# Kernel tuning notes

Hardware: AMD Instinct MI355X
Metric: run time of the kernel (lower is better)

## Reference

```python
import jax, jax.numpy as jnp
import numpy as np

B, H, S, D = 2, 16, 2048, 64

def setup_inputs() -> dict:
    key = jax.random.key(0)
    kq, kk, kv = jax.random.split(key, 3)
    Q = jax.random.normal(kq, (B, H, S, D), dtype=jnp.float32)
    K = jax.random.normal(kk, (B, H, S, D), dtype=jnp.float32)
    V = jax.random.normal(kv, (B, H, S, D), dtype=jnp.float32)
    # causal mask, broadcastable over batch/head dims (True = keep)
    mask = jnp.tril(jnp.ones((S, S), dtype=jnp.bool_))
    return {"Q": Q, "K": K, "V": V, "mask": mask}

def reference(Q, K, V, mask):
    scale = jax.lax.rsqrt(jnp.float32(Q.shape[-1]))
    # [b, h, q, k] attention logits
    at = jnp.einsum('bhqd,bhkd->bhqk', Q, K) * scale
    at = jnp.where(mask, at, -jnp.inf)
    # manual numerically-stable softmax (matches SoftMax module)
    x_max = jnp.max(at, axis=-1, keepdims=True)
    x_exp = jnp.exp(at - x_max)
    scores = x_exp / jnp.sum(x_exp, axis=-1, keepdims=True)
    return jnp.einsum('bhqk,bhkd->bhqd', scores, V)
```

## Files before the change

kernel.cpp:

```cpp
#include <hip/hip_runtime.h>
#include <math.h>

typedef __attribute__((ext_vector_type(8))) short bf16x8;
typedef __attribute__((ext_vector_type(8))) short s16x8;
typedef __attribute__((ext_vector_type(4))) short s16x4;
typedef __attribute__((ext_vector_type(4))) int   i32x4;
typedef __attribute__((ext_vector_type(4))) float f32x4;
typedef __attribute__((ext_vector_type(16))) float f32x16;

namespace {
constexpr int kS   = 2048;
constexpr int kD   = 64;
constexpr int kBH  = 32;
constexpr int kT   = kS / 64;
constexpr int PPAD = 72;
constexpr float kScaleLog2e = 0.125f * 1.44269504088896340736f;
}

__device__ __forceinline__ short f2bf(float f) {
    union { float f; unsigned u; } c; c.f = f;
    unsigned r = c.u + 0x7fffu + ((c.u >> 16) & 1u);
    return (short)(r >> 16);
}

__device__ __forceinline__ s16x8 pack8(const float4& a, const float4& b) {
    s16x8 r;
    r[0] = f2bf(a.x); r[1] = f2bf(a.y); r[2] = f2bf(a.z); r[3] = f2bf(a.w);
    r[4] = f2bf(b.x); r[5] = f2bf(b.y); r[6] = f2bf(b.z); r[7] = f2bf(b.w);
    return r;
}

__device__ __forceinline__ float hexp2(float x) {
    float r;
    asm("v_exp_f32 %0, %1" : "=v"(r) : "v"(x));
    return r;
}

__device__ __forceinline__ unsigned cvtpk(float lo, float hi_) {
    unsigned r;
    asm("v_cvt_pk_bf16_f32 %0, %1, %2" : "=v"(r) : "v"(lo), "v"(hi_));
    return r;
}
__device__ __forceinline__ void plswap(unsigned& a, unsigned& b) {
    asm("v_permlane32_swap_b32 %0, %1" : "+v"(a), "+v"(b));
}

__global__ __launch_bounds__(256)
void prepack(const float* __restrict__ K, const float* __restrict__ V,
             short* __restrict__ wsK, short* __restrict__ wsVT)
{
    __shared__ float vt[64][65];
    const int tid = threadIdx.x;
    const int kb  = blockIdx.x;
    const int bh  = blockIdx.y;
    const int r   = tid >> 2;
    const int s   = tid & 3;
    const int c0  = s * 16;

    const size_t grow = ((size_t)bh * kS + (size_t)kb * 64 + r) * kD + c0;
    const size_t tbase = ((size_t)bh * kT + kb) * 4096;

    {
        const float4* kr = (const float4*)(K + grow);
        float4 a = kr[0], b = kr[1], c = kr[2], d = kr[3];
        const int kt = r >> 5, ql = r & 31;
        short* out = wsK + tbase + (size_t)((s * 2 + kt) * 64) * 8;
        *(s16x8*)(out + (size_t)ql * 8)        = pack8(a, b);
        *(s16x8*)(out + (size_t)(32 + ql) * 8) = pack8(c, d);
    }
    {
        const float4* vr = (const float4*)(V + grow);
        float4 a = vr[0], b = vr[1], c = vr[2], d = vr[3];
        float t[16] = {a.x,a.y,a.z,a.w, b.x,b.y,b.z,b.w,
                       c.x,c.y,c.z,c.w, d.x,d.y,d.z,d.w};
        #pragma unroll
        for (int jj = 0; jj < 16; ++jj) vt[r][c0 + jj] = t[jj];
    }
    __syncthreads();
    {
        const int d     = tid >> 2;
        const int slice = tid & 3;
        const int k0    = slice * 16;
        const int dt = d >> 5, ql = d & 31;
        s16x8 g0, g1;
        #pragma unroll
        for (int jj = 0; jj < 8; ++jj) g0[jj] = f2bf(vt[k0 + jj][d]);
        #pragma unroll
        for (int jj = 0; jj < 8; ++jj) g1[jj] = f2bf(vt[k0 + 8 + jj][d]);
        short* out = wsVT + tbase + (size_t)((slice * 2 + dt) * 64) * 8;
        *(s16x8*)(out + (size_t)ql * 8)        = g0;
        *(s16x8*)(out + (size_t)(32 + ql) * 8) = g1;
    }
}

__global__ __launch_bounds__(64)
void attn_v11(const float* __restrict__ Q, const short* __restrict__ wsK,
              const short* __restrict__ wsVT, float* __restrict__ O)
{
    const int lane = threadIdx.x & 63;
    const int ql   = lane & 31;
    const int hi   = lane >> 5;

    const int n    = (int)blockIdx.x;
    const int xcd  = n & 7;
    const int rest = n >> 3;
    const int bh   = xcd * 4 + (rest >> 5);
    const int p    = rest & 31;

    const char* Kroot = (const char*)wsK + (size_t)bh * kT * 8192;
    const char* Vroot = (const char*)wsVT + (size_t)bh * kT * 8192;

    f32x16 z16;
    #pragma unroll
    for (int c = 0; c < 16; ++c) z16[c] = 0.f;

    bf16x8 onesA;
    #pragma unroll
    for (int i = 0; i < 8; ++i) onesA[i] = (short)0x3F80;

    auto loadK = [&](int kb, bf16x8 (&kf)[8]) {
        const char* kp = Kroot + (size_t)kb * 8192 + lane * 16;
        #pragma unroll
        for (int i = 0; i < 8; ++i)
            kf[i] = *(const bf16x8*)(kp + i * 1024);
    };

    #pragma unroll 1
    for (int sidx = 0; sidx < 2; ++sidx) {
        const int qs   = sidx == 0 ? 63 - p : p;
        const int T    = (qs >> 1) + 1;
        const int qrow = qs * 32 + ql;

        const float* Qr = Q + ((size_t)bh * kS + qrow) * kD;
        bf16x8 qf[4];
        #pragma unroll
        for (int s = 0; s < 4; ++s) {
            const float4 a = *(const float4*)(Qr + s * 16 + hi * 8);
            const float4 b = *(const float4*)(Qr + s * 16 + hi * 8 + 4);
            bf16x8 f;
            f[0] = f2bf(a.x * kScaleLog2e); f[1] = f2bf(a.y * kScaleLog2e);
            f[2] = f2bf(a.z * kScaleLog2e); f[3] = f2bf(a.w * kScaleLog2e);
            f[4] = f2bf(b.x * kScaleLog2e); f[5] = f2bf(b.y * kScaleLog2e);
            f[6] = f2bf(b.z * kScaleLog2e); f[7] = f2bf(b.w * kScaleLog2e);
            qf[s] = f;
        }

        f32x16 o[2] = {z16, z16};
        f32x16 lacc = z16;

        bf16x8 kA[8], kB[8];
        loadK(0, kA);

        auto tile = [&](bf16x8 (&kcur)[8], bf16x8 (&knxt)[8], int kb) {
            bf16x8 vf[8];
            {
                const char* vp = Vroot + (size_t)kb * 8192 + lane * 16;
                #pragma unroll
                for (int i = 0; i < 8; ++i)
                    vf[i] = *(const bf16x8*)(vp + i * 1024);
            }

            f32x16 sacc[2];
            #pragma unroll
            for (int kt = 0; kt < 2; ++kt) {
                sacc[kt] = __builtin_amdgcn_mfma_f32_32x32x16_bf16(
                    kcur[kt], qf[0], z16, 0, 0, 0);
                #pragma unroll
                for (int s = 1; s < 4; ++s)
                    sacc[kt] = __builtin_amdgcn_mfma_f32_32x32x16_bf16(
                        kcur[s * 2 + kt], qf[s], sacc[kt], 0, 0, 0);
            }

            if (kb + 1 < T) loadK(kb + 1, knxt);

            if (kb == T - 1) {
                #pragma unroll
                for (int kt = 0; kt < 2; ++kt) {
                    const int kbase = kb * 64 + kt * 32 + 4 * hi;
                    #pragma unroll
                    for (int c = 0; c < 16; ++c) {
                        const int kg = kbase + (c & 3) + 8 * (c >> 2);
                        if (kg > qrow) sacc[kt][c] = -1e30f;
                    }
                }
            }

            #pragma unroll
            for (int kt = 0; kt < 2; ++kt)
                #pragma unroll
                for (int c = 0; c < 16; ++c)
                    sacc[kt][c] = hexp2(sacc[kt][c]);

            #pragma unroll
            for (int kt = 0; kt < 2; ++kt) {
                unsigned w8[8];
                #pragma unroll
                for (int i = 0; i < 8; ++i)
                    w8[i] = cvtpk(sacc[kt][2 * i], sacc[kt][2 * i + 1]);
                #pragma unroll
                for (int s = 0; s < 2; ++s) {
                    unsigned A0 = w8[4 * s + 0], B0 = w8[4 * s + 2];
                    unsigned A1 = w8[4 * s + 1], B1 = w8[4 * s + 3];
                    plswap(A0, B0);
                    plswap(A1, B1);
                    i32x4 wv;
                    wv[0] = (int)A0; wv[1] = (int)A1;
                    wv[2] = (int)B0; wv[3] = (int)B1;
                    const bf16x8 pv = __builtin_bit_cast(bf16x8, wv);
                    #pragma unroll
                    for (int dt = 0; dt < 2; ++dt)
                        o[dt] = __builtin_amdgcn_mfma_f32_32x32x16_bf16(
                            vf[(kt * 2 + s) * 2 + dt], pv, o[dt], 0, 0, 0);
                    lacc = __builtin_amdgcn_mfma_f32_32x32x16_bf16(
                        onesA, pv, lacc, 0, 0, 0);
                }
            }
        };

        int kb = 0;
        #pragma unroll 1
        while (true) {
            tile(kA, kB, kb);
            if (++kb == T) break;
            tile(kB, kA, kb);
            if (++kb == T) break;
        }

        const float inv = 1.0f / lacc[0];
        float* Ob = O + ((size_t)bh * kS + qrow) * kD;
        #pragma unroll
        for (int dt = 0; dt < 2; ++dt)
            #pragma unroll
            for (int t = 0; t < 4; ++t) {
                float4 v;
                v.x = o[dt][4 * t + 0] * inv;
                v.y = o[dt][4 * t + 1] * inv;
                v.z = o[dt][4 * t + 2] * inv;
                v.w = o[dt][4 * t + 3] * inv;
                *(float4*)(Ob + dt * 32 + 4 * hi + 8 * t) = v;
            }
    }
}

__global__ __launch_bounds__(256)
void attn_mfma(const float* __restrict__ Q, const float* __restrict__ K,
               const float* __restrict__ V, float* __restrict__ O)
{
    __shared__ short Klds[64 * PPAD];
    __shared__ short VTlds[64 * PPAD];
    __shared__ short Plds[4 * 16 * PPAD];

    const int tid  = threadIdx.x;
    const int lane = tid & 63;
    const int w    = tid >> 6;
    const int lo   = lane & 15;
    const int hi   = lane >> 4;
    const int qt = (int)gridDim.x - 1 - (int)blockIdx.x;
    const int bh = blockIdx.y;
    const size_t hbase = (size_t)bh * kS * kD;

    const float* Qr = Q + hbase + (size_t)(qt * 64 + w * 16 + lo) * kD;
    bf16x8 qfrag[2];
    #pragma unroll
    for (int dc = 0; dc < 2; ++dc) {
        const float4 a = *(const float4*)(Qr + dc * 32 + hi * 8);
        const float4 b = *(const float4*)(Qr + dc * 32 + hi * 8 + 4);
        bf16x8 f;
        f[0] = f2bf(a.x * kScaleLog2e); f[1] = f2bf(a.y * kScaleLog2e);
        f[2] = f2bf(a.z * kScaleLog2e); f[3] = f2bf(a.w * kScaleLog2e);
        f[4] = f2bf(b.x * kScaleLog2e); f[5] = f2bf(b.y * kScaleLog2e);
        f[6] = f2bf(b.z * kScaleLog2e); f[7] = f2bf(b.w * kScaleLog2e);
        qfrag[dc] = f;
    }

    const f32x4 zero4 = {0.f, 0.f, 0.f, 0.f};
    f32x4 o[4] = {zero4, zero4, zero4, zero4};
    float m_[4] = {-1e30f, -1e30f, -1e30f, -1e30f};
    float l_[4] = {0.f, 0.f, 0.f, 0.f};
    const int sr = tid >> 2;
    const int sc = (tid & 3) * 16;
    const float* Kg = K + hbase;
    const float* Vg = V + hbase;
    short* Pw = &Plds[w * 16 * PPAD];

    for (int kb = 0; kb <= qt; ++kb) {
        __syncthreads();
        {
            const float* krow = Kg + (size_t)(kb * 64 + sr) * kD + sc;
            const float* vrow = Vg + (size_t)(kb * 64 + sr) * kD + sc;
            #pragma unroll
            for (int i = 0; i < 4; ++i) {
                const float4 kv = ((const float4*)krow)[i];
                s16x4 ks;
                ks[0] = f2bf(kv.x); ks[1] = f2bf(kv.y);
                ks[2] = f2bf(kv.z); ks[3] = f2bf(kv.w);
                *(s16x4*)&Klds[sr * PPAD + sc + i * 4] = ks;
                const float4 vv = ((const float4*)vrow)[i];
                VTlds[(sc + i * 4 + 0) * PPAD + sr] = f2bf(vv.x);
                VTlds[(sc + i * 4 + 1) * PPAD + sr] = f2bf(vv.y);
                VTlds[(sc + i * 4 + 2) * PPAD + sr] = f2bf(vv.z);
                VTlds[(sc + i * 4 + 3) * PPAD + sr] = f2bf(vv.w);
            }
        }
        __syncthreads();

        f32x4 sacc[4] = {zero4, zero4, zero4, zero4};
        #pragma unroll
        for (int kk = 0; kk < 4; ++kk)
            #pragma unroll
            for (int dc = 0; dc < 2; ++dc) {
                const bf16x8 kf = *(const bf16x8*)(
                    &Klds[(kk * 16 + lo) * PPAD + dc * 32 + hi * 8]);
                sacc[kk] = __builtin_amdgcn_mfma_f32_16x16x32_bf16(
                    qfrag[dc], kf, sacc[kk], 0, 0, 0);
            }
        if (kb == qt) {
            #pragma unroll
            for (int kk = 0; kk < 4; ++kk)
                #pragma unroll
                for (int r = 0; r < 4; ++r)
                    if (kk * 16 + lo > w * 16 + hi * 4 + r) sacc[kk][r] = -1e30f;
        }
        float nm[4], alpha[4];
        #pragma unroll
        for (int r = 0; r < 4; ++r) {
            float v = fmaxf(fmaxf(sacc[0][r], sacc[1][r]),
                            fmaxf(sacc[2][r], sacc[3][r]));
            v = fmaxf(v, __shfl_xor(v, 1));
            v = fmaxf(v, __shfl_xor(v, 2));
            v = fmaxf(v, __shfl_xor(v, 4));
            v = fmaxf(v, __shfl_xor(v, 8));
            nm[r]    = fmaxf(v, m_[r]);
            alpha[r] = exp2f(m_[r] - nm[r]);
        }
        float p[4][4];
        #pragma unroll
        for (int kk = 0; kk < 4; ++kk)
            #pragma unroll
            for (int r = 0; r < 4; ++r)
                p[kk][r] = exp2f(sacc[kk][r] - nm[r]);
        #pragma unroll
        for (int r = 0; r < 4; ++r) {
            float s = (p[0][r] + p[1][r]) + (p[2][r] + p[3][r]);
            s += __shfl_xor(s, 1);
            s += __shfl_xor(s, 2);
            s += __shfl_xor(s, 4);
            s += __shfl_xor(s, 8);
            l_[r] = l_[r] * alpha[r] + s;
            m_[r] = nm[r];
        }
        #pragma unroll
        for (int dcB = 0; dcB < 4; ++dcB)
            #pragma unroll
            for (int r = 0; r < 4; ++r)
                o[dcB][r] *= alpha[r];
        #pragma unroll
        for (int kk = 0; kk < 4; ++kk)
            #pragma unroll
            for (int r = 0; r < 4; ++r)
                Pw[(hi * 4 + r) * PPAD + kk * 16 + lo] = f2bf(p[kk][r]);
        #pragma unroll
        for (int kc = 0; kc < 2; ++kc) {
            const bf16x8 pf = *(const bf16x8*)(&Pw[lo * PPAD + kc * 32 + hi * 8]);
            #pragma unroll
            for (int dcB = 0; dcB < 4; ++dcB) {
                const bf16x8 vf = *(const bf16x8*)(
                    &VTlds[(dcB * 16 + lo) * PPAD + kc * 32 + hi * 8]);
                o[dcB] = __builtin_amdgcn_mfma_f32_16x16x32_bf16(
                    pf, vf, o[dcB], 0, 0, 0);
            }
        }
    }
    float* Ob = O + hbase;
    #pragma unroll
    for (int r = 0; r < 4; ++r) {
        const float inv = 1.0f / l_[r];
        const size_t q = (size_t)(qt * 64 + w * 16 + hi * 4 + r);
        #pragma unroll
        for (int dcB = 0; dcB < 4; ++dcB)
            Ob[q * kD + dcB * 16 + lo] = o[dcB][r] * inv;
    }
}

extern "C" void kernel_launch(void* const* d_in, const int* in_sizes, int n_in,
                              void* d_out, int out_size, void* d_ws, size_t ws_size,
                              hipStream_t stream) {
    const float* Q = (const float*)d_in[0];
    const float* K = (const float*)d_in[1];
    const float* V = (const float*)d_in[2];
    float* out = (float*)d_out;
    (void)in_sizes; (void)n_in; (void)out_size;

    const size_t elemsK   = (size_t)kBH * kS * kD;
    const size_t need_pre = elemsK * 2 * sizeof(short);

    if (ws_size >= need_pre) {
        short* wsK  = (short*)d_ws;
        short* wsVT = wsK + elemsK;
        prepack<<<dim3(kT, kBH), 256, 0, stream>>>(K, V, wsK, wsVT);
        attn_v11<<<dim3(1024), 64, 0, stream>>>(Q, wsK, wsVT, out);
    } else {
        attn_mfma<<<dim3(kT, kBH), 256, 0, stream>>>(Q, K, V, out);
    }
}
```

Before: 52.13 us.

## Share K/V tiles across four waves via LDS with async global-to-LDS staging

Replaces the one-wave-per-block attention kernel with a 256-thread block of four waves covering 128 query rows. These waves share double-buffered K/V tiles that are loaded into LDS with global_load_lds. This cuts redundant global/L2 traffic for K and V by a factor of four and overlaps the next tile's load with compute. The cost is a __syncthreads per key tile and only 256 blocks instead of 1024. The causal mask check is also generalised per wave, because waves in a block end their causal range at different points.

```diff
diff --git a/kernel.cpp b/kernel.cpp
--- a/kernel.cpp
+++ b/kernel.cpp
@@ -43,6 +43,12 @@
 }
 __device__ __forceinline__ void plswap(unsigned& a, unsigned& b) {
     asm("v_permlane32_swap_b32 %0, %1" : "+v"(a), "+v"(b));
+}
+
+typedef const __attribute__((address_space(1))) void* gas_t;
+typedef __attribute__((address_space(3))) void* las_t;
+__device__ __forceinline__ void glds16(const void* g, void* l) {
+    __builtin_amdgcn_global_load_lds((gas_t)g, (las_t)l, 16, 0, 0);
 }
 
 __global__ __launch_bounds__(256)
@@ -93,19 +99,24 @@
     }
 }
 
-__global__ __launch_bounds__(64)
-void attn_v11(const float* __restrict__ Q, const short* __restrict__ wsK,
+__global__ __launch_bounds__(256)
+void attn_v12(const float* __restrict__ Q, const short* __restrict__ wsK,
               const short* __restrict__ wsVT, float* __restrict__ O)
 {
-    const int lane = threadIdx.x & 63;
+    __shared__ short Kst[2][4096];
+    __shared__ short Vst[2][4096];
+
+    const int tid  = threadIdx.x;
+    const int lane = tid & 63;
+    const int w    = tid >> 6;
     const int ql   = lane & 31;
     const int hi   = lane >> 5;
 
-    const int n    = (int)blockIdx.x;
-    const int xcd  = n & 7;
-    const int rest = n >> 3;
-    const int bh   = xcd * 4 + (rest >> 5);
-    const int p    = rest & 31;
+    const int n   = (int)blockIdx.x;
+    const int xcd = n & 7;
+    const int j   = n >> 3;
+    const int bh  = xcd * 4 + (j & 3);
+    const int pr  = j >> 2;
 
     const char* Kroot = (const char*)wsK + (size_t)bh * kT * 8192;
     const char* Vroot = (const char*)wsVT + (size_t)bh * kT * 8192;
@@ -118,18 +129,22 @@
     #pragma unroll
     for (int i = 0; i < 8; ++i) onesA[i] = (short)0x3F80;
 
-    auto loadK = [&](int kb, bf16x8 (&kf)[8]) {
-        const char* kp = Kroot + (size_t)kb * 8192 + lane * 16;
-        #pragma unroll
-        for (int i = 0; i < 8; ++i)
-            kf[i] = *(const bf16x8*)(kp + i * 1024);
+    auto stage = [&](int kb, int b) {
+        const char* ks = Kroot + (size_t)kb * 8192 + tid * 16;
+        const char* vs = Vroot + (size_t)kb * 8192 + tid * 16;
+        char* kl = (char*)&Kst[b][0] + tid * 16;
+        char* vl = (char*)&Vst[b][0] + tid * 16;
+        glds16(ks,        kl);
+        glds16(ks + 4096, kl + 4096);
+        glds16(vs,        vl);
+        glds16(vs + 4096, vl + 4096);
     };
 
     #pragma unroll 1
-    for (int sidx = 0; sidx < 2; ++sidx) {
-        const int qs   = sidx == 0 ? 63 - p : p;
-        const int T    = (qs >> 1) + 1;
-        const int qrow = qs * 32 + ql;
+    for (int ph = 0; ph < 2; ++ph) {
+        const int qb   = ph ? pr : (15 - pr);
+        const int T    = 2 * qb + 2;
+        const int qrow = qb * 128 + w * 32 + ql;
 
         const float* Qr = Q + ((size_t)bh * kS + qrow) * kD;
         bf16x8 qf[4];
@@ -148,32 +163,32 @@
         f32x16 o[2] = {z16, z16};
         f32x16 lacc = z16;
 
-        bf16x8 kA[8], kB[8];
-        loadK(0, kA);
-
-        auto tile = [&](bf16x8 (&kcur)[8], bf16x8 (&knxt)[8], int kb) {
-            bf16x8 vf[8];
-            {
-                const char* vp = Vroot + (size_t)kb * 8192 + lane * 16;
-                #pragma unroll
-                for (int i = 0; i < 8; ++i)
-                    vf[i] = *(const bf16x8*)(vp + i * 1024);
-            }
+        stage(0, 0);
+        __syncthreads();
+
+        #pragma unroll 1
+        for (int kb = 0; kb < T; ++kb) {
+            const int b = kb & 1;
+            if (kb + 1 < T) stage(kb + 1, b ^ 1);
+
+            const char* Kl = (const char*)&Kst[b][0] + lane * 16;
+            const char* Vl = (const char*)&Vst[b][0] + lane * 16;
 
             f32x16 sacc[2];
             #pragma unroll
             for (int kt = 0; kt < 2; ++kt) {
+                const bf16x8 k0 = *(const bf16x8*)(Kl + kt * 1024);
                 sacc[kt] = __builtin_amdgcn_mfma_f32_32x32x16_bf16(
-                    kcur[kt], qf[0], z16, 0, 0, 0);
-                #pragma unroll
-                for (int s = 1; s < 4; ++s)
+                    k0, qf[0], z16, 0, 0, 0);
+                #pragma unroll
+                for (int s = 1; s < 4; ++s) {
+                    const bf16x8 kf = *(const bf16x8*)(Kl + (s * 2 + kt) * 1024);
                     sacc[kt] = __builtin_amdgcn_mfma_f32_32x32x16_bf16(
-                        kcur[s * 2 + kt], qf[s], sacc[kt], 0, 0, 0);
-            }
-
-            if (kb + 1 < T) loadK(kb + 1, knxt);
-
-            if (kb == T - 1) {
+                        kf, qf[s], sacc[kt], 0, 0, 0);
+                }
+            }
+
+            if (kb * 64 + 63 > qrow) {
                 #pragma unroll
                 for (int kt = 0; kt < 2; ++kt) {
                     const int kbase = kb * 64 + kt * 32 + 4 * hi;
@@ -208,22 +223,18 @@
                     wv[2] = (int)B0; wv[3] = (int)B1;
                     const bf16x8 pv = __builtin_bit_cast(bf16x8, wv);
                     #pragma unroll
-                    for (int dt = 0; dt < 2; ++dt)
+                    for (int dt = 0; dt < 2; ++dt) {
+                        const bf16x8 vfr = *(const bf16x8*)(
+                            Vl + ((kt * 2 + s) * 2 + dt) * 1024);
                         o[dt] = __builtin_amdgcn_mfma_f32_32x32x16_bf16(
-                            vf[(kt * 2 + s) * 2 + dt], pv, o[dt], 0, 0, 0);
+                            vfr, pv, o[dt], 0, 0, 0);
+                    }
                     lacc = __builtin_amdgcn_mfma_f32_32x32x16_bf16(
                         onesA, pv, lacc, 0, 0, 0);
                 }
             }
-        };
-
-        int kb = 0;
-        #pragma unroll 1
-        while (true) {
-            tile(kA, kB, kb);
-            if (++kb == T) break;
-            tile(kB, kA, kb);
-            if (++kb == T) break;
+
+            __syncthreads();
         }
 
         const float inv = 1.0f / lacc[0];
@@ -239,6 +250,7 @@
                 v.w = o[dt][4 * t + 3] * inv;
                 *(float4*)(Ob + dt * 32 + 4 * hi + 8 * t) = v;
             }
+        __syncthreads();
     }
 }
 
@@ -398,7 +410,7 @@
         short* wsK  = (short*)d_ws;
         short* wsVT = wsK + elemsK;
         prepack<<<dim3(kT, kBH), 256, 0, stream>>>(K, V, wsK, wsVT);
-        attn_v11<<<dim3(1024), 64, 0, stream>>>(Q, wsK, wsVT, out);
+        attn_v12<<<dim3(256), 256, 0, stream>>>(Q, wsK, wsVT, out);
     } else {
         attn_mfma<<<dim3(kT, kBH), 256, 0, stream>>>(Q, K, V, out);
     }
```

Result: slower. 58.28 us (+11.8%).

## Software-pipeline QK^T one tile ahead and double-buffer V loads with MFMA priority

Applied to the files above, without the earlier changes.

Restructures the attention inner loop so the QK^T MFMAs for tile kb+1 are issued before the softmax and PV work of tile kb. K is now prefetched two tiles ahead and V one tile ahead, each into its own double buffer. s_setprio is raised around MFMA groups so matrix work gets issue priority over other waves. This aims to hide global-load latency and the exp/convert ALU work behind MFMA, at the cost of more VGPRs for the extra S and V buffers, which could reduce occupancy or cause spills.

```diff
diff --git a/kernel.cpp b/kernel.cpp
--- a/kernel.cpp
+++ b/kernel.cpp
@@ -94,7 +94,7 @@
 }
 
 __global__ __launch_bounds__(64)
-void attn_v11(const float* __restrict__ Q, const short* __restrict__ wsK,
+void attn_v13(const float* __restrict__ Q, const short* __restrict__ wsK,
               const short* __restrict__ wsVT, float* __restrict__ O)
 {
     const int lane = threadIdx.x & 63;
@@ -123,6 +123,12 @@
         #pragma unroll
         for (int i = 0; i < 8; ++i)
             kf[i] = *(const bf16x8*)(kp + i * 1024);
+    };
+    auto loadV = [&](int kb, bf16x8 (&vf)[8]) {
+        const char* vp = Vroot + (size_t)kb * 8192 + lane * 16;
+        #pragma unroll
+        for (int i = 0; i < 8; ++i)
+            vf[i] = *(const bf16x8*)(vp + i * 1024);
     };
 
     #pragma unroll 1
@@ -148,31 +154,21 @@
         f32x16 o[2] = {z16, z16};
         f32x16 lacc = z16;
 
-        bf16x8 kA[8], kB[8];
-        loadK(0, kA);
-
-        auto tile = [&](bf16x8 (&kcur)[8], bf16x8 (&knxt)[8], int kb) {
-            bf16x8 vf[8];
-            {
-                const char* vp = Vroot + (size_t)kb * 8192 + lane * 16;
-                #pragma unroll
-                for (int i = 0; i < 8; ++i)
-                    vf[i] = *(const bf16x8*)(vp + i * 1024);
-            }
-
-            f32x16 sacc[2];
+        auto qkt = [&](bf16x8 (&kf)[8], f32x16 (&S)[2]) {
+            __builtin_amdgcn_s_setprio(1);
             #pragma unroll
             for (int kt = 0; kt < 2; ++kt) {
-                sacc[kt] = __builtin_amdgcn_mfma_f32_32x32x16_bf16(
-                    kcur[kt], qf[0], z16, 0, 0, 0);
+                S[kt] = __builtin_amdgcn_mfma_f32_32x32x16_bf16(
+                    kf[kt], qf[0], z16, 0, 0, 0);
                 #pragma unroll
                 for (int s = 1; s < 4; ++s)
-                    sacc[kt] = __builtin_amdgcn_mfma_f32_32x32x16_bf16(
-                        kcur[s * 2 + kt], qf[s], sacc[kt], 0, 0, 0);
-            }
-
-            if (kb + 1 < T) loadK(kb + 1, knxt);
-
+                    S[kt] = __builtin_amdgcn_mfma_f32_32x32x16_bf16(
+                        kf[s * 2 + kt], qf[s], S[kt], 0, 0, 0);
+            }
+            __builtin_amdgcn_s_setprio(0);
+        };
+
+        auto finish = [&](f32x16 (&S)[2], bf16x8 (&vf)[8], int kb) {
             if (kb == T - 1) {
                 #pragma unroll
                 for (int kt = 0; kt < 2; ++kt) {
@@ -180,23 +176,22 @@
                     #pragma unroll
                     for (int c = 0; c < 16; ++c) {
                         const int kg = kbase + (c & 3) + 8 * (c >> 2);
-                        if (kg > qrow) sacc[kt][c] = -1e30f;
+                        if (kg > qrow) S[kt][c] = -1e30f;
                     }
                 }
             }
-
             #pragma unroll
             for (int kt = 0; kt < 2; ++kt)
                 #pragma unroll
                 for (int c = 0; c < 16; ++c)
-                    sacc[kt][c] = hexp2(sacc[kt][c]);
+                    S[kt][c] = hexp2(S[kt][c]);
 
             #pragma unroll
             for (int kt = 0; kt < 2; ++kt) {
                 unsigned w8[8];
                 #pragma unroll
                 for (int i = 0; i < 8; ++i)
-                    w8[i] = cvtpk(sacc[kt][2 * i], sacc[kt][2 * i + 1]);
+                    w8[i] = cvtpk(S[kt][2 * i], S[kt][2 * i + 1]);
                 #pragma unroll
                 for (int s = 0; s < 2; ++s) {
                     unsigned A0 = w8[4 * s + 0], B0 = w8[4 * s + 2];
@@ -207,22 +202,39 @@
                     wv[0] = (int)A0; wv[1] = (int)A1;
                     wv[2] = (int)B0; wv[3] = (int)B1;
                     const bf16x8 pv = __builtin_bit_cast(bf16x8, wv);
+                    __builtin_amdgcn_s_setprio(1);
                     #pragma unroll
                     for (int dt = 0; dt < 2; ++dt)
                         o[dt] = __builtin_amdgcn_mfma_f32_32x32x16_bf16(
                             vf[(kt * 2 + s) * 2 + dt], pv, o[dt], 0, 0, 0);
                     lacc = __builtin_amdgcn_mfma_f32_32x32x16_bf16(
                         onesA, pv, lacc, 0, 0, 0);
+                    __builtin_amdgcn_s_setprio(0);
                 }
             }
         };
+
+        bf16x8 kA[8], kB[8], vA[8], vB[8];
+        f32x16 Sa[2], Sb[2];
+
+        loadK(0, kA);
+        loadV(0, vA);
+        qkt(kA, Sa);
+        if (T > 1) loadK(1, kB);
 
         int kb = 0;
         #pragma unroll 1
         while (true) {
-            tile(kA, kB, kb);
+            if (kb + 1 < T) qkt(kB, Sb);
+            if (kb + 2 < T) loadK(kb + 2, kA);
+            if (kb + 1 < T) loadV(kb + 1, vB);
+            finish(Sa, vA, kb);
             if (++kb == T) break;
-            tile(kB, kA, kb);
+
+            if (kb + 1 < T) qkt(kA, Sa);
+            if (kb + 2 < T) loadK(kb + 2, kB);
+            if (kb + 1 < T) loadV(kb + 1, vA);
+            finish(Sb, vB, kb);
             if (++kb == T) break;
         }
 
@@ -398,7 +410,7 @@
         short* wsK  = (short*)d_ws;
         short* wsVT = wsK + elemsK;
         prepack<<<dim3(kT, kBH), 256, 0, stream>>>(K, V, wsK, wsVT);
-        attn_v11<<<dim3(1024), 64, 0, stream>>>(Q, wsK, wsVT, out);
+        attn_v13<<<dim3(1024), 64, 0, stream>>>(Q, wsK, wsVT, out);
     } else {
         attn_mfma<<<dim3(kT, kBH), 256, 0, stream>>>(Q, K, V, out);
     }
```

After: 54.18 us. +3.9%, slower.
